# Performance work log

Hardware: AMD Instinct MI355X
Metric: run time of the kernel (lower is better)

## Reference

```python
import jax, jax.numpy as jnp
import numpy as np

N = 100000
E = 3200000
G = 2000
H = 128
NODE_DIM = 11
L = 4


def setup_inputs() -> dict:
    key = jax.random.key(0)
    ks = jax.random.split(key, 20)
    x = jax.random.normal(ks[0], (N, NODE_DIM), dtype=jnp.float32)
    pos = jax.random.normal(ks[1], (N, 3), dtype=jnp.float32)
    edge_index = jax.random.randint(ks[2], (2, E), 0, N, dtype=jnp.int64)
    batch = jnp.sort(jax.random.randint(ks[3], (N,), 0, G, dtype=jnp.int64))
    s = 0.05
    emb_W = jax.random.normal(ks[4], (NODE_DIM, H), dtype=jnp.float32) * s
    emb_b = jnp.zeros((H,), dtype=jnp.float32)
    edge_w1 = jax.random.normal(ks[5], (L, 2 * H + 1, H), dtype=jnp.float32) * s
    edge_b1 = jnp.zeros((L, H), dtype=jnp.float32)
    edge_w2 = jax.random.normal(ks[6], (L, H, H), dtype=jnp.float32) * s
    edge_b2 = jnp.zeros((L, H), dtype=jnp.float32)
    node_w = jax.random.normal(ks[7], (L, 2 * H, H), dtype=jnp.float32) * s
    node_b = jnp.zeros((L, H), dtype=jnp.float32)
    coord_w = jax.random.normal(ks[8], (L, H, 1), dtype=jnp.float32) * s
    coord_b = jnp.zeros((L, 1), dtype=jnp.float32)
    head_w1 = jax.random.normal(ks[9], (H, H), dtype=jnp.float32) * s
    head_b1 = jnp.zeros((H,), dtype=jnp.float32)
    head_w2 = jax.random.normal(ks[10], (H, 1), dtype=jnp.float32) * s
    head_b2 = jnp.zeros((1,), dtype=jnp.float32)
    return {"x": x, "pos": pos, "edge_index": edge_index, "batch": batch,
            "emb_W": emb_W, "emb_b": emb_b,
            "edge_w1": edge_w1, "edge_b1": edge_b1,
            "edge_w2": edge_w2, "edge_b2": edge_b2,
            "node_w": node_w, "node_b": node_b,
            "coord_w": coord_w, "coord_b": coord_b,
            "head_w1": head_w1, "head_b1": head_b1,
            "head_w2": head_w2, "head_b2": head_b2}


def reference(x, pos, edge_index, batch, emb_W, emb_b,
              edge_w1, edge_b1, edge_w2, edge_b2,
              node_w, node_b, coord_w, coord_b,
              head_w1, head_b1, head_w2, head_b2):
    silu = jax.nn.silu
    row = edge_index[0]
    col = edge_index[1]
    h = x @ emb_W + emb_b  # [N, H]
    for l in range(L):
        diff = pos[row] - pos[col]                         # [E, 3]
        dist2 = jnp.sum(diff * diff, axis=1, keepdims=True)  # [E, 1]
        ef = jnp.concatenate([h[row], h[col], dist2], axis=1)  # [E, 2H+1]
        m = silu(ef @ edge_w1[l] + edge_b1[l])
        m = silu(m @ edge_w2[l] + edge_b2[l])               # [E, H]
        coord_update = diff * jnp.tanh(m @ coord_w[l] + coord_b[l])  # [E, 3]
        pos = pos + jax.ops.segment_sum(coord_update, row, num_segments=N)
        agg = jax.ops.segment_sum(m, row, num_segments=N)   # [N, H]
        h = silu(jnp.concatenate([h, agg], axis=1) @ node_w[l] + node_b[l])
    # global mean pool
    sums = jax.ops.segment_sum(h, batch, num_segments=G)    # [G, H]
    counts = jax.ops.segment_sum(jnp.ones((h.shape[0],), h.dtype), batch, num_segments=G)
    pooled = sums / jnp.maximum(counts, 1.0)[:, None]
    out = silu(pooled @ head_w1 + head_b1) @ head_w2 + head_b2  # [G, 1]
    return out.squeeze(-1)
```

## Files before the change

kernel.cpp:

```cpp
#include <hip/hip_runtime.h>
#include <math.h>

#define HDIM 128
#define ET 64
#define KC 32
#define MSTR 264

typedef __attribute__((ext_vector_type(8))) short short8;
typedef __attribute__((ext_vector_type(4))) float f32x4;

__device__ __forceinline__ float silu_f(float x) {
    return x / (1.0f + __expf(-x));
}
__device__ __forceinline__ unsigned short f2bf(float f) {
    unsigned int u = __float_as_uint(f);
    u = (u + 0x7FFF + ((u >> 16) & 1)) >> 16;
    return (unsigned short)u;
}
__device__ __forceinline__ float bf2f(unsigned short v) {
    return __uint_as_float(((unsigned int)v) << 16);
}

__global__ __launch_bounds__(256) void embed_kernel(
    const float* __restrict__ x, const float* __restrict__ W,
    const float* __restrict__ b, float* __restrict__ h,
    unsigned short* __restrict__ hbf, int N)
{
    int n = blockIdx.x * 2 + (threadIdx.x >> 7);
    int j = threadIdx.x & 127;
    if (n >= N) return;
    float s = b[j];
#pragma unroll
    for (int k = 0; k < 11; ++k) s += x[n * 11 + k] * W[k * HDIM + j];
    h[(size_t)n * HDIM + j] = s;
    hbf[(size_t)n * HDIM + j] = f2bf(s);
}

__global__ __launch_bounds__(256) void count_kernel(
    const int* __restrict__ row, int* __restrict__ cnt, int E)
{
    int e = blockIdx.x * 256 + threadIdx.x;
    if (e < E) atomicAdd(&cnt[row[e]], 1);
}

__global__ __launch_bounds__(1024) void scan_kernel(
    const int* __restrict__ cnt, int* __restrict__ cursor, int Nn)
{
    __shared__ int lds[1024];
    int t = threadIdx.x;
    int chunk = (Nn + 1023) >> 10;
    int base = t * chunk;
    int s = 0;
    for (int k = 0; k < chunk; ++k) {
        int n = base + k;
        if (n < Nn) s += cnt[n];
    }
    lds[t] = s;
    __syncthreads();
    for (int d = 1; d < 1024; d <<= 1) {
        int v = (t >= d) ? lds[t - d] : 0;
        __syncthreads();
        lds[t] += v;
        __syncthreads();
    }
    int run = lds[t] - s;
    for (int k = 0; k < chunk; ++k) {
        int n = base + k;
        if (n < Nn) { cursor[n] = run; run += cnt[n]; }
    }
}

__global__ __launch_bounds__(256) void scatter_kernel(
    const int* __restrict__ row, const int* __restrict__ col,
    int* __restrict__ cursor, int* __restrict__ srow, int* __restrict__ scol, int E)
{
    int e = blockIdx.x * 256 + threadIdx.x;
    if (e < E) {
        int r = row[e];
        int p = atomicAdd(&cursor[r], 1);
        srow[p] = r;
        scol[p] = col[e];
    }
}

__global__ __launch_bounds__(256) void pack_w1_kernel(
    const float* __restrict__ ew1, unsigned short* __restrict__ w1p)
{
    int idx = blockIdx.x * 256 + threadIdx.x;
    int l    = idx >> 12;
    int kt   = (idx >> 9) & 7;
    int ct   = (idx >> 6) & 7;
    int lane = idx & 63;
    const float* src = ew1 + (size_t)l * 257 * HDIM;
    short8 hi, lo;
#pragma unroll
    for (int j = 0; j < 8; ++j) {
        float w = src[(size_t)(kt * 32 + (lane >> 4) * 8 + j) * HDIM + ct * 16 + (lane & 15)];
        unsigned short h = f2bf(w);
        hi[j] = (short)h;
        lo[j] = (short)f2bf(w - bf2f(h));
    }
    size_t base = (size_t)l * 65536;
    *(short8*)(w1p + base + ((size_t)((kt * 2 + 0) * 8 + ct) * 64 + lane) * 8) = hi;
    *(short8*)(w1p + base + ((size_t)((kt * 2 + 1) * 8 + ct) * 64 + lane) * 8) = lo;
}

__global__ __launch_bounds__(256) void pack_w2_kernel(
    const float* __restrict__ ew2, unsigned short* __restrict__ w2p)
{
    int idx = blockIdx.x * 256 + threadIdx.x;
    int l    = idx >> 11;
    int kt   = (idx >> 9) & 3;
    int ct   = (idx >> 6) & 7;
    int lane = idx & 63;
    const float* src = ew2 + (size_t)l * HDIM * HDIM;
    short8 hi, lo;
#pragma unroll
    for (int j = 0; j < 8; ++j) {
        float w = src[(size_t)(kt * 32 + (lane >> 4) * 8 + j) * HDIM + ct * 16 + (lane & 15)];
        unsigned short h = f2bf(w);
        hi[j] = (short)h;
        lo[j] = (short)f2bf(w - bf2f(h));
    }
    size_t base = (size_t)l * 32768;
    *(short8*)(w2p + base + ((size_t)((kt * 2 + 0) * 8 + ct) * 64 + lane) * 8) = hi;
    *(short8*)(w2p + base + ((size_t)((kt * 2 + 1) * 8 + ct) * 64 + lane) * 8) = lo;
}

__global__ __launch_bounds__(256, 2) void edge_kernel(
    const unsigned short* __restrict__ hbf,
    const float* __restrict__ pos,
    const int*   __restrict__ row,
    const int*   __restrict__ col,
    const unsigned short* __restrict__ w1p,
    const float* __restrict__ w1r256,
    const float* __restrict__ b1,
    const unsigned short* __restrict__ w2p,
    const float* __restrict__ b2,
    const float* __restrict__ cw,
    const float* __restrict__ cb,
    float* __restrict__ agg,
    float* __restrict__ posn)
{
    __shared__ __align__(16) short Wbuf[2][4096];
    __shared__ __align__(16) short m1lds[ET * MSTR];
    __shared__ float diff_lds[3][ET];
    __shared__ float dist2_lds[ET];
    __shared__ int   row_lds[ET];
    __shared__ int   col_lds[ET];

    const int tid  = threadIdx.x;
    const int lane = tid & 63;
    const int wv   = tid >> 6;
    const long long e0 = (long long)blockIdx.x * ET;

    if (tid < ET) {
        long long e = e0 + tid;
        int r = row[e], c = col[e];
        row_lds[tid] = r; col_lds[tid] = c;
        float dx = pos[r * 3 + 0] - pos[c * 3 + 0];
        float dy = pos[r * 3 + 1] - pos[c * 3 + 1];
        float dz = pos[r * 3 + 2] - pos[c * 3 + 2];
        diff_lds[0][tid] = dx; diff_lds[1][tid] = dy; diff_lds[2][tid] = dz;
        dist2_lds[tid] = dx * dx + dy * dy + dz * dz;
    }
    __syncthreads();

    const int e16  = wv * 16 + (lane & 15);
    const int ksub = (lane >> 4) * 8;
    const int r_i  = row_lds[e16];
    const int c_i  = col_lds[e16];
    short8 afrag[8];
#pragma unroll
    for (int kt = 0; kt < 8; ++kt) {
        int idx = (kt < 4) ? r_i : c_i;
        afrag[kt] = *(const short8*)(hbf + (size_t)idx * HDIM + (kt & 3) * 32 + ksub);
    }

    f32x4 acc[8];
#pragma unroll
    for (int ct = 0; ct < 8; ++ct) acc[ct] = (f32x4){0.f, 0.f, 0.f, 0.f};

    {
        const int4* s = (const int4*)w1p;
        int4* d = (int4*)Wbuf[0];
        d[tid] = s[tid]; d[tid + 256] = s[tid + 256];
    }
    __syncthreads();
    for (int vt = 0; vt < 16; ++vt) {
        const int cur = vt & 1;
        int4 r0, r1;
        if (vt < 15) {
            const int4* s = (const int4*)(w1p + (size_t)(vt + 1) * 4096);
            r0 = s[tid]; r1 = s[tid + 256];
        }
        const int kt = vt >> 1;
#pragma unroll
        for (int ct = 0; ct < 8; ++ct) {
            short8 b = *(const short8*)&Wbuf[cur][ct * 512 + lane * 8];
            acc[ct] = __builtin_amdgcn_mfma_f32_16x16x32_bf16(afrag[kt], b, acc[ct], 0, 0, 0);
        }
        if (vt < 15) {
            int4* d = (int4*)Wbuf[cur ^ 1];
            d[tid] = r0; d[tid + 256] = r1;
        }
        __syncthreads();
    }

    {
        const int cbase = lane & 15;
        const int ebase = wv * 16 + (lane >> 4) * 4;
        float w256v[8], b1v[8];
#pragma unroll
        for (int ct = 0; ct < 8; ++ct) {
            w256v[ct] = w1r256[ct * 16 + cbase];
            b1v[ct]   = b1[ct * 16 + cbase];
        }
        float d2v[4];
#pragma unroll
        for (int r_ = 0; r_ < 4; ++r_) d2v[r_] = dist2_lds[ebase + r_];
#pragma unroll
        for (int ct = 0; ct < 8; ++ct)
#pragma unroll
            for (int r_ = 0; r_ < 4; ++r_) {
                float v = silu_f(acc[ct][r_] + d2v[r_] * w256v[ct] + b1v[ct]);
                m1lds[(ebase + r_) * MSTR + ct * 16 + cbase] = (short)f2bf(v);
            }
    }
    __syncthreads();

    short8 a2[4];
#pragma unroll
    for (int kt = 0; kt < 4; ++kt)
        a2[kt] = *(const short8*)&m1lds[e16 * MSTR + kt * 32 + ksub];

    f32x4 acc2[8];
#pragma unroll
    for (int ct = 0; ct < 8; ++ct) acc2[ct] = (f32x4){0.f, 0.f, 0.f, 0.f};

    {
        const int4* s = (const int4*)w2p;
        int4* d = (int4*)Wbuf[0];
        d[tid] = s[tid]; d[tid + 256] = s[tid + 256];
    }
    __syncthreads();
    for (int vt = 0; vt < 8; ++vt) {
        const int cur = vt & 1;
        int4 r0, r1;
        if (vt < 7) {
            const int4* s = (const int4*)(w2p + (size_t)(vt + 1) * 4096);
            r0 = s[tid]; r1 = s[tid + 256];
        }
        const int kt = vt >> 1;
#pragma unroll
        for (int ct = 0; ct < 8; ++ct) {
            short8 b = *(const short8*)&Wbuf[cur][ct * 512 + lane * 8];
            acc2[ct] = __builtin_amdgcn_mfma_f32_16x16x32_bf16(a2[kt], b, acc2[ct], 0, 0, 0);
        }
        if (vt < 7) {
            int4* d = (int4*)Wbuf[cur ^ 1];
            d[tid] = r0; d[tid + 256] = r1;
        }
        __syncthreads();
    }

    float* mfl = (float*)m1lds;
    {
        const int cbase = lane & 15;
        const int ebase = wv * 16 + (lane >> 4) * 4;
        float b2v[8], cwv8[8];
#pragma unroll
        for (int ct = 0; ct < 8; ++ct) {
            b2v[ct]  = b2[ct * 16 + cbase];
            cwv8[ct] = cw[ct * 16 + cbase];
        }
        float part[4] = {0.f, 0.f, 0.f, 0.f};
#pragma unroll
        for (int ct = 0; ct < 8; ++ct)
#pragma unroll
            for (int r_ = 0; r_ < 4; ++r_) {
                float v = silu_f(acc2[ct][r_] + b2v[ct]);
                acc2[ct][r_] = v;
                part[r_] += v * cwv8[ct];
            }
#pragma unroll
        for (int d = 8; d >= 1; d >>= 1)
#pragma unroll
            for (int r_ = 0; r_ < 4; ++r_) part[r_] += __shfl_xor(part[r_], d);

        if (cbase == 0) {
            float cbv = cb[0];
#pragma unroll
            for (int r_ = 0; r_ < 4; ++r_) {
                int el = ebase + r_;
                float t = tanhf(part[r_] + cbv);
                diff_lds[0][el] *= t;
                diff_lds[1][el] *= t;
                diff_lds[2][el] *= t;
            }
        }
#pragma unroll
        for (int ct = 0; ct < 8; ++ct)
#pragma unroll
            for (int r_ = 0; r_ < 4; ++r_)
                mfl[(ebase + r_) * 132 + ct * 16 + cbase] = acc2[ct][r_];
    }
    __syncthreads();

    {
        int j    = tid & 127;
        int half = tid >> 7;
        int eb   = half * 32;
        float a  = 0.0f;
        int prev = row_lds[eb];
#pragma unroll 8
        for (int e = eb; e < eb + 32; ++e) {
            int r = row_lds[e];
            if (r != prev) {
                atomicAdd(&agg[(size_t)prev * HDIM + j], a);
                a = 0.0f; prev = r;
            }
            a += mfl[e * 132 + j];
        }
        atomicAdd(&agg[(size_t)prev * HDIM + j], a);
    }
    if (tid < 3) {
        int d = tid;
        float a = 0.0f;
        int prev = row_lds[0];
        for (int e = 0; e < ET; ++e) {
            int r = row_lds[e];
            if (r != prev) {
                atomicAdd(&posn[(size_t)prev * 3 + d], a);
                a = 0.0f; prev = r;
            }
            a += diff_lds[d][e];
        }
        atomicAdd(&posn[(size_t)prev * 3 + d], a);
    }
}

__global__ __launch_bounds__(256, 2) void node_kernel(
    const float* __restrict__ h, const float* __restrict__ agg,
    const float* __restrict__ W,
    const float* __restrict__ nb,
    float* __restrict__ hout, unsigned short* __restrict__ houtbf, int N)
{
    __shared__ float Wlds[KC * HDIM];
    __shared__ float abuf[ET * 36];

    const int tid = threadIdx.x;
    const int n0 = blockIdx.x * ET;
    const int jq8 = (tid & 15) * 8;
    const int eg4 = (tid >> 4) * 4;
    const int gl_e = tid >> 2;
    const int gl_k = (tid & 3) * 8;

    float acc[4][8];
#pragma unroll
    for (int i = 0; i < 4; ++i)
#pragma unroll
        for (int j = 0; j < 8; ++j) acc[i][j] = 0.0f;

    for (int c = 0; c < 8; ++c) {
        {
            const float4* src = (const float4*)(W + (size_t)c * KC * HDIM);
            float4* dst = (float4*)Wlds;
#pragma unroll
            for (int t = 0; t < 4; ++t) dst[tid + t * 256] = src[tid + t * 256];
        }
        {
            int n = n0 + gl_e;
            int koff = (c & 3) * KC;
            float4* adst = (float4*)(abuf + gl_e * 36 + gl_k);
            if (n < N) {
                const float* base = (c < 4) ? h : agg;
                const float4* asrc = (const float4*)(base + (size_t)n * HDIM + koff + gl_k);
                adst[0] = asrc[0]; adst[1] = asrc[1];
            } else {
                float4 z = make_float4(0.f, 0.f, 0.f, 0.f);
                adst[0] = z; adst[1] = z;
            }
        }
        __syncthreads();
#pragma unroll 8
        for (int kk = 0; kk < KC; ++kk) {
            float a0 = abuf[(eg4 + 0) * 36 + kk];
            float a1 = abuf[(eg4 + 1) * 36 + kk];
            float a2 = abuf[(eg4 + 2) * 36 + kk];
            float a3 = abuf[(eg4 + 3) * 36 + kk];
            float4 w0 = *(const float4*)&Wlds[kk * HDIM + jq8];
            float4 w1 = *(const float4*)&Wlds[kk * HDIM + jq8 + 4];
            float w[8] = {w0.x, w0.y, w0.z, w0.w, w1.x, w1.y, w1.z, w1.w};
            float a[4] = {a0, a1, a2, a3};
#pragma unroll
            for (int i = 0; i < 4; ++i)
#pragma unroll
                for (int j = 0; j < 8; ++j) acc[i][j] += a[i] * w[j];
        }
        __syncthreads();
    }

    float bb[8];
    *(float4*)&bb[0] = *(const float4*)(nb + jq8);
    *(float4*)&bb[4] = *(const float4*)(nb + jq8 + 4);
#pragma unroll
    for (int i = 0; i < 4; ++i) {
        int n = n0 + eg4 + i;
        if (n < N) {
            float v[8];
#pragma unroll
            for (int j = 0; j < 8; ++j) v[j] = silu_f(acc[i][j] + bb[j]);
            *(float4*)(hout + (size_t)n * HDIM + jq8)     = make_float4(v[0], v[1], v[2], v[3]);
            *(float4*)(hout + (size_t)n * HDIM + jq8 + 4) = make_float4(v[4], v[5], v[6], v[7]);
            unsigned short* hb = houtbf + (size_t)n * HDIM + jq8;
#pragma unroll
            for (int j = 0; j < 8; ++j) hb[j] = f2bf(v[j]);
        }
    }
}

__global__ __launch_bounds__(256) void pool_kernel(
    const float* __restrict__ h, const int* __restrict__ batch,
    float* __restrict__ pooled, float* __restrict__ cnt, int N)
{
    int idx = blockIdx.x * 256 + threadIdx.x;
    int n = idx >> 5;
    int jg = idx & 31;
    if (n >= N) return;
    int b = batch[n];
    float4 v = *(const float4*)(h + (size_t)n * HDIM + jg * 4);
    atomicAdd(&pooled[(size_t)b * HDIM + jg * 4 + 0], v.x);
    atomicAdd(&pooled[(size_t)b * HDIM + jg * 4 + 1], v.y);
    atomicAdd(&pooled[(size_t)b * HDIM + jg * 4 + 2], v.z);
    atomicAdd(&pooled[(size_t)b * HDIM + jg * 4 + 3], v.w);
    if (jg == 0) atomicAdd(&cnt[b], 1.0f);
}

__global__ __launch_bounds__(128) void head_kernel(
    const float* __restrict__ pooled, const float* __restrict__ cnt,
    const float* __restrict__ W1, const float* __restrict__ b1,
    const float* __restrict__ w2, const float* __restrict__ b2,
    float* __restrict__ out)
{
    __shared__ float p[HDIM];
    __shared__ float red[2];
    int g = blockIdx.x, j = threadIdx.x;
    float c = fmaxf(cnt[g], 1.0f);
    p[j] = pooled[(size_t)g * HDIM + j] / c;
    __syncthreads();
    float s = b1[j];
#pragma unroll 8
    for (int k = 0; k < HDIM; ++k) s += p[k] * W1[k * HDIM + j];
    float contrib = silu_f(s) * w2[j];
#pragma unroll
    for (int d = 32; d >= 1; d >>= 1) contrib += __shfl_xor(contrib, d);
    if ((j & 63) == 0) red[j >> 6] = contrib;
    __syncthreads();
    if (j == 0) out[g] = red[0] + red[1] + b2[0];
}

extern "C" void kernel_launch(void* const* d_in, const int* in_sizes, int n_in,
                              void* d_out, int out_size, void* d_ws, size_t ws_size,
                              hipStream_t stream)
{
    const float* x      = (const float*)d_in[0];
    const float* pos_in = (const float*)d_in[1];
    const int*   ei     = (const int*)d_in[2];
    const int*   batch  = (const int*)d_in[3];
    const float* emb_W  = (const float*)d_in[4];
    const float* emb_b  = (const float*)d_in[5];
    const float* ew1    = (const float*)d_in[6];
    const float* eb1    = (const float*)d_in[7];
    const float* ew2    = (const float*)d_in[8];
    const float* eb2    = (const float*)d_in[9];
    const float* nw     = (const float*)d_in[10];
    const float* nb     = (const float*)d_in[11];
    const float* cwv    = (const float*)d_in[12];
    const float* cbv    = (const float*)d_in[13];
    const float* hw1    = (const float*)d_in[14];
    const float* hb1    = (const float*)d_in[15];
    const float* hw2    = (const float*)d_in[16];
    const float* hb2    = (const float*)d_in[17];
    float* out = (float*)d_out;

    const int N = in_sizes[0] / 11;
    const int E = in_sizes[2] / 2;
    const int G = out_size;
    const int* row = ei;
    const int* col = ei + E;

    float* ws = (float*)d_ws;
    float* hA     = ws;
    float* hB     = hA  + (size_t)N * HDIM;
    float* agg    = hB  + (size_t)N * HDIM;
    float* hbf_f  = agg + (size_t)N * HDIM;
    unsigned short* hbf = (unsigned short*)hbf_f;
    float* w1p_f  = hbf_f + (size_t)N * 64;
    unsigned short* w1p = (unsigned short*)w1p_f;
    float* w2p_f  = w1p_f + 131072;
    unsigned short* w2p = (unsigned short*)w2p_f;
    float* posA   = w2p_f + 65536;
    float* posB   = posA + (size_t)N * 3;
    float* pooled = posB + (size_t)N * 3;
    float* cnt    = pooled + (size_t)G * HDIM;
    int*   srow   = (int*)(cnt + G);
    int*   scol   = srow + E;
    int*   cntN   = scol + E;
    int*   curN   = cntN + N;

    hipMemsetAsync(cntN, 0, (size_t)N * sizeof(int), stream);
    count_kernel<<<(E + 255) / 256, 256, 0, stream>>>(row, cntN, E);
    scan_kernel<<<1, 1024, 0, stream>>>(cntN, curN, N);
    scatter_kernel<<<(E + 255) / 256, 256, 0, stream>>>(row, col, curN, srow, scol, E);

    pack_w1_kernel<<<64, 256, 0, stream>>>(ew1, w1p);
    pack_w2_kernel<<<32, 256, 0, stream>>>(ew2, w2p);

    embed_kernel<<<(N + 1) / 2, 256, 0, stream>>>(x, emb_W, emb_b, hA, hbf, N);

    const float* hcur = hA;
    float* hnext = hB;
    const float* pcur = pos_in;
    float* pbufs[2] = {posA, posB};

    for (int l = 0; l < 4; ++l) {
        float* pn = pbufs[l & 1];
        hipMemsetAsync(agg, 0, (size_t)N * HDIM * sizeof(float), stream);
        hipMemcpyAsync(pn, pcur, (size_t)N * 3 * sizeof(float),
                       hipMemcpyDeviceToDevice, stream);
        edge_kernel<<<E / ET, 256, 0, stream>>>(
            hbf, pcur, srow, scol,
            w1p + (size_t)l * 65536,
            ew1 + (size_t)l * 257 * HDIM + 256 * HDIM,
            eb1 + (size_t)l * HDIM,
            w2p + (size_t)l * 32768,
            eb2 + (size_t)l * HDIM,
            cwv + (size_t)l * HDIM, cbv + l,
            agg, pn);
        node_kernel<<<(N + ET - 1) / ET, 256, 0, stream>>>(
            hcur, agg, nw + (size_t)l * 256 * HDIM, nb + (size_t)l * HDIM,
            hnext, hbf, N);
        const float* th = hcur; hcur = hnext; hnext = (float*)th;
        pcur = pn;
    }

    hipMemsetAsync(pooled, 0, (size_t)G * (HDIM + 1) * sizeof(float), stream);
    pool_kernel<<<(N * 32 + 255) / 256, 256, 0, stream>>>(hcur, batch, pooled, cnt, N);
    head_kernel<<<G, 128, 0, stream>>>(pooled, cnt, hw1, hb1, hw2, hb2, out);
}
```

Baseline: 6.878 ms.

## Split edge MLP output columns across waves and read weights from global directly

The edge kernel now assigns each wave 32 output columns over all 64 edges, instead of 16 edges over all 128 columns. Weight fragments are loaded straight from global or L2 into registers, which removes the LDS double-buffer staging and its per-step barriers. Occupancy is raised to 4 blocks per SM. The coordinate dot product is now reduced across waves through a small shared array. The risks are more gather loads of h rows per wave (each wave fetches all 64 edges' features), repeated weight reads from cache, and register pressure under the tighter launch bound.

```diff
diff --git a/kernel.cpp b/kernel.cpp
--- a/kernel.cpp
+++ b/kernel.cpp
@@ -127,7 +127,7 @@
     *(short8*)(w2p + base + ((size_t)((kt * 2 + 1) * 8 + ct) * 64 + lane) * 8) = lo;
 }
 
-__global__ __launch_bounds__(256, 2) void edge_kernel(
+__global__ __launch_bounds__(256, 4) void edge_kernel(
     const unsigned short* __restrict__ hbf,
     const float* __restrict__ pos,
     const int*   __restrict__ row,
@@ -142,16 +142,18 @@
     float* __restrict__ agg,
     float* __restrict__ posn)
 {
-    __shared__ __align__(16) short Wbuf[2][4096];
     __shared__ __align__(16) short m1lds[ET * MSTR];
     __shared__ float diff_lds[3][ET];
     __shared__ float dist2_lds[ET];
+    __shared__ float pdot[4][ET];
     __shared__ int   row_lds[ET];
     __shared__ int   col_lds[ET];
 
     const int tid  = threadIdx.x;
     const int lane = tid & 63;
     const int wv   = tid >> 6;
+    const int cbase = lane & 15;
+    const int kgrp  = lane >> 4;
     const long long e0 = (long long)blockIdx.x * ET;
 
     if (tid < ET) {
@@ -166,146 +168,119 @@
     }
     __syncthreads();
 
-    const int e16  = wv * 16 + (lane & 15);
-    const int ksub = (lane >> 4) * 8;
-    const int r_i  = row_lds[e16];
-    const int c_i  = col_lds[e16];
-    short8 afrag[8];
+    int ridx[4], cidx[4];
+#pragma unroll
+    for (int ea = 0; ea < 4; ++ea) {
+        ridx[ea] = row_lds[ea * 16 + cbase];
+        cidx[ea] = col_lds[ea * 16 + cbase];
+    }
+
+    f32x4 acc[4][2];
+#pragma unroll
+    for (int ea = 0; ea < 4; ++ea)
+#pragma unroll
+        for (int ci = 0; ci < 2; ++ci) acc[ea][ci] = (f32x4){0.f, 0.f, 0.f, 0.f};
+
 #pragma unroll
     for (int kt = 0; kt < 8; ++kt) {
-        int idx = (kt < 4) ? r_i : c_i;
-        afrag[kt] = *(const short8*)(hbf + (size_t)idx * HDIM + (kt & 3) * 32 + ksub);
-    }
-
-    f32x4 acc[8];
-#pragma unroll
-    for (int ct = 0; ct < 8; ++ct) acc[ct] = (f32x4){0.f, 0.f, 0.f, 0.f};
+        short8 a[4];
+#pragma unroll
+        for (int ea = 0; ea < 4; ++ea) {
+            int idx = (kt < 4) ? ridx[ea] : cidx[ea];
+            a[ea] = *(const short8*)(hbf + (size_t)idx * HDIM + (kt & 3) * 32 + kgrp * 8);
+        }
+#pragma unroll
+        for (int ph = 0; ph < 2; ++ph) {
+            short8 bA = *(const short8*)(w1p + ((size_t)((kt * 2 + ph) * 8 + wv * 2 + 0) * 64 + lane) * 8);
+            short8 bB = *(const short8*)(w1p + ((size_t)((kt * 2 + ph) * 8 + wv * 2 + 1) * 64 + lane) * 8);
+#pragma unroll
+            for (int ea = 0; ea < 4; ++ea) {
+                acc[ea][0] = __builtin_amdgcn_mfma_f32_16x16x32_bf16(a[ea], bA, acc[ea][0], 0, 0, 0);
+                acc[ea][1] = __builtin_amdgcn_mfma_f32_16x16x32_bf16(a[ea], bB, acc[ea][1], 0, 0, 0);
+            }
+        }
+    }
 
     {
-        const int4* s = (const int4*)w1p;
-        int4* d = (int4*)Wbuf[0];
-        d[tid] = s[tid]; d[tid + 256] = s[tid + 256];
-    }
-    __syncthreads();
-    for (int vt = 0; vt < 16; ++vt) {
-        const int cur = vt & 1;
-        int4 r0, r1;
-        if (vt < 15) {
-            const int4* s = (const int4*)(w1p + (size_t)(vt + 1) * 4096);
-            r0 = s[tid]; r1 = s[tid + 256];
-        }
-        const int kt = vt >> 1;
-#pragma unroll
-        for (int ct = 0; ct < 8; ++ct) {
-            short8 b = *(const short8*)&Wbuf[cur][ct * 512 + lane * 8];
-            acc[ct] = __builtin_amdgcn_mfma_f32_16x16x32_bf16(afrag[kt], b, acc[ct], 0, 0, 0);
-        }
-        if (vt < 15) {
-            int4* d = (int4*)Wbuf[cur ^ 1];
-            d[tid] = r0; d[tid + 256] = r1;
-        }
-        __syncthreads();
-    }
-
-    {
-        const int cbase = lane & 15;
-        const int ebase = wv * 16 + (lane >> 4) * 4;
-        float w256v[8], b1v[8];
-#pragma unroll
-        for (int ct = 0; ct < 8; ++ct) {
-            w256v[ct] = w1r256[ct * 16 + cbase];
-            b1v[ct]   = b1[ct * 16 + cbase];
-        }
-        float d2v[4];
-#pragma unroll
-        for (int r_ = 0; r_ < 4; ++r_) d2v[r_] = dist2_lds[ebase + r_];
-#pragma unroll
-        for (int ct = 0; ct < 8; ++ct)
-#pragma unroll
-            for (int r_ = 0; r_ < 4; ++r_) {
-                float v = silu_f(acc[ct][r_] + d2v[r_] * w256v[ct] + b1v[ct]);
-                m1lds[(ebase + r_) * MSTR + ct * 16 + cbase] = (short)f2bf(v);
+        float w256v[2], b1v[2];
+#pragma unroll
+        for (int ci = 0; ci < 2; ++ci) {
+            int c = wv * 32 + ci * 16 + cbase;
+            w256v[ci] = w1r256[c];
+            b1v[ci]   = b1[c];
+        }
+#pragma unroll
+        for (int ea = 0; ea < 4; ++ea)
+#pragma unroll
+            for (int ci = 0; ci < 2; ++ci)
+#pragma unroll
+                for (int rr = 0; rr < 4; ++rr) {
+                    int e = ea * 16 + kgrp * 4 + rr;
+                    float v = silu_f(acc[ea][ci][rr] + dist2_lds[e] * w256v[ci] + b1v[ci]);
+                    m1lds[e * MSTR + wv * 32 + ci * 16 + cbase] = (short)f2bf(v);
+                }
+    }
+    __syncthreads();
+
+    f32x4 acc2[4][2];
+#pragma unroll
+    for (int ea = 0; ea < 4; ++ea)
+#pragma unroll
+        for (int ci = 0; ci < 2; ++ci) acc2[ea][ci] = (f32x4){0.f, 0.f, 0.f, 0.f};
+
+#pragma unroll
+    for (int kt = 0; kt < 4; ++kt) {
+        short8 a[4];
+#pragma unroll
+        for (int ea = 0; ea < 4; ++ea)
+            a[ea] = *(const short8*)&m1lds[(ea * 16 + cbase) * MSTR + kt * 32 + kgrp * 8];
+#pragma unroll
+        for (int ph = 0; ph < 2; ++ph) {
+            short8 bA = *(const short8*)(w2p + ((size_t)((kt * 2 + ph) * 8 + wv * 2 + 0) * 64 + lane) * 8);
+            short8 bB = *(const short8*)(w2p + ((size_t)((kt * 2 + ph) * 8 + wv * 2 + 1) * 64 + lane) * 8);
+#pragma unroll
+            for (int ea = 0; ea < 4; ++ea) {
+                acc2[ea][0] = __builtin_amdgcn_mfma_f32_16x16x32_bf16(a[ea], bA, acc2[ea][0], 0, 0, 0);
+                acc2[ea][1] = __builtin_amdgcn_mfma_f32_16x16x32_bf16(a[ea], bB, acc2[ea][1], 0, 0, 0);
             }
-    }
-    __syncthreads();
-
-    short8 a2[4];
-#pragma unroll
-    for (int kt = 0; kt < 4; ++kt)
-        a2[kt] = *(const short8*)&m1lds[e16 * MSTR + kt * 32 + ksub];
-
-    f32x4 acc2[8];
-#pragma unroll
-    for (int ct = 0; ct < 8; ++ct) acc2[ct] = (f32x4){0.f, 0.f, 0.f, 0.f};
-
-    {
-        const int4* s = (const int4*)w2p;
-        int4* d = (int4*)Wbuf[0];
-        d[tid] = s[tid]; d[tid + 256] = s[tid + 256];
-    }
-    __syncthreads();
-    for (int vt = 0; vt < 8; ++vt) {
-        const int cur = vt & 1;
-        int4 r0, r1;
-        if (vt < 7) {
-            const int4* s = (const int4*)(w2p + (size_t)(vt + 1) * 4096);
-            r0 = s[tid]; r1 = s[tid + 256];
-        }
-        const int kt = vt >> 1;
-#pragma unroll
-        for (int ct = 0; ct < 8; ++ct) {
-            short8 b = *(const short8*)&Wbuf[cur][ct * 512 + lane * 8];
-            acc2[ct] = __builtin_amdgcn_mfma_f32_16x16x32_bf16(a2[kt], b, acc2[ct], 0, 0, 0);
-        }
-        if (vt < 7) {
-            int4* d = (int4*)Wbuf[cur ^ 1];
-            d[tid] = r0; d[tid + 256] = r1;
-        }
-        __syncthreads();
-    }
+        }
+    }
+    __syncthreads();
 
     float* mfl = (float*)m1lds;
     {
-        const int cbase = lane & 15;
-        const int ebase = wv * 16 + (lane >> 4) * 4;
-        float b2v[8], cwv8[8];
-#pragma unroll
-        for (int ct = 0; ct < 8; ++ct) {
-            b2v[ct]  = b2[ct * 16 + cbase];
-            cwv8[ct] = cw[ct * 16 + cbase];
-        }
-        float part[4] = {0.f, 0.f, 0.f, 0.f};
-#pragma unroll
-        for (int ct = 0; ct < 8; ++ct)
-#pragma unroll
-            for (int r_ = 0; r_ < 4; ++r_) {
-                float v = silu_f(acc2[ct][r_] + b2v[ct]);
-                acc2[ct][r_] = v;
-                part[r_] += v * cwv8[ct];
+        float b2v[2], cwv2[2];
+#pragma unroll
+        for (int ci = 0; ci < 2; ++ci) {
+            int c = wv * 32 + ci * 16 + cbase;
+            b2v[ci]  = b2[c];
+            cwv2[ci] = cw[c];
+        }
+#pragma unroll
+        for (int ea = 0; ea < 4; ++ea)
+#pragma unroll
+            for (int rr = 0; rr < 4; ++rr) {
+                int e = ea * 16 + kgrp * 4 + rr;
+                float p = 0.f;
+#pragma unroll
+                for (int ci = 0; ci < 2; ++ci) {
+                    float v = silu_f(acc2[ea][ci][rr] + b2v[ci]);
+                    mfl[e * 132 + wv * 32 + ci * 16 + cbase] = v;
+                    p += v * cwv2[ci];
+                }
+#pragma unroll
+                for (int d = 8; d >= 1; d >>= 1) p += __shfl_xor(p, d);
+                if (cbase == 0) pdot[wv][e] = p;
             }
-#pragma unroll
-        for (int d = 8; d >= 1; d >>= 1)
-#pragma unroll
-            for (int r_ = 0; r_ < 4; ++r_) part[r_] += __shfl_xor(part[r_], d);
-
-        if (cbase == 0) {
-            float cbv = cb[0];
-#pragma unroll
-            for (int r_ = 0; r_ < 4; ++r_) {
-                int el = ebase + r_;
-                float t = tanhf(part[r_] + cbv);
-                diff_lds[0][el] *= t;
-                diff_lds[1][el] *= t;
-                diff_lds[2][el] *= t;
-            }
-        }
-#pragma unroll
-        for (int ct = 0; ct < 8; ++ct)
-#pragma unroll
-            for (int r_ = 0; r_ < 4; ++r_)
-                mfl[(ebase + r_) * 132 + ct * 16 + cbase] = acc2[ct][r_];
-    }
-    __syncthreads();
+    }
+    __syncthreads();
+
+    if (tid < ET) {
+        float t = tanhf(pdot[0][tid] + pdot[1][tid] + pdot[2][tid] + pdot[3][tid] + cb[0]);
+        diff_lds[0][tid] *= t;
+        diff_lds[1][tid] *= t;
+        diff_lds[2][tid] *= t;
+    }
 
     {
         int j    = tid & 127;
@@ -324,6 +299,7 @@
         }
         atomicAdd(&agg[(size_t)prev * HDIM + j], a);
     }
+    __syncthreads();
     if (tid < 3) {
         int d = tid;
         float a = 0.0f;
```

Measured after the change: 5.830 ms. 15.2% less time.
